# Performance work log

Hardware: AMD Instinct MI355X
Metric: run time of the kernel (lower is better)

Reference implementation:

```python
import jax, jax.numpy as jnp
import numpy as np

EMBED_DIM = 1024
NUM_HEADS = 16
HEAD_DIM = EMBED_DIM // NUM_HEADS
SEQ_LEN = 2048
BATCH = 2


def setup_inputs() -> dict:
    key = jax.random.key(0)
    ks = jax.random.split(key, 9)
    s = 1.0 / np.sqrt(EMBED_DIM)
    inputs = jax.random.normal(ks[0], (BATCH, SEQ_LEN, EMBED_DIM), dtype=jnp.float32)
    Wq = jax.random.uniform(ks[1], (EMBED_DIM, EMBED_DIM), jnp.float32, -s, s)
    bq = jax.random.uniform(ks[2], (EMBED_DIM,), jnp.float32, -s, s)
    Wk = jax.random.uniform(ks[3], (EMBED_DIM, EMBED_DIM), jnp.float32, -s, s)
    bk = jax.random.uniform(ks[4], (EMBED_DIM,), jnp.float32, -s, s)
    Wv = jax.random.uniform(ks[5], (EMBED_DIM, EMBED_DIM), jnp.float32, -s, s)
    bv = jax.random.uniform(ks[6], (EMBED_DIM,), jnp.float32, -s, s)
    Wo = jax.random.uniform(ks[7], (EMBED_DIM, EMBED_DIM), jnp.float32, -s, s)
    bo = jax.random.uniform(ks[8], (EMBED_DIM,), jnp.float32, -s, s)
    return {"inputs": inputs, "Wq": Wq, "bq": bq, "Wk": Wk, "bk": bk,
            "Wv": Wv, "bv": bv, "Wo": Wo, "bo": bo}


def reference(inputs, Wq, bq, Wk, bk, Wv, bv, Wo, bo):
    B, S, D = inputs.shape
    H, Hd = NUM_HEADS, HEAD_DIM

    def heads(x):  # [B,S,D] -> [B,H,S,Hd]
        return x.reshape(B, S, H, Hd).transpose(0, 2, 1, 3)

    q = heads(inputs @ Wq + bq)
    k = heads(inputs @ Wk + bk)
    v = heads(inputs @ Wv + bv)

    # [B,H,S,S] causal scores (naive, matching original module)
    scores = jnp.einsum('bhqd,bhkd->bhqk', q, k) * (Hd ** -0.5)
    causal = jnp.tril(jnp.ones((S, S), dtype=bool))
    scores = jnp.where(causal, scores, jnp.float32(-jnp.inf))
    attn = jax.nn.softmax(scores, axis=-1)

    out = jnp.einsum('bhqk,bhkd->bhqd', attn, v)
    out = out.transpose(0, 2, 1, 3).reshape(B, S, D)
    return out @ Wo + bo
```

## Files before the change

### kernel.cpp

```cpp
#include <hip/hip_runtime.h>
#include <stdint.h>
#include <stddef.h>

#define SEQ   2048
#define DIM   1024
#define NH    16
#define HD    64
#define MTOT  4096
#define LPAD  72
#define EPAD  136
#define FPAD  132

typedef __attribute__((ext_vector_type(8))) short short8;
typedef __attribute__((ext_vector_type(4))) float floatx4;
typedef __attribute__((ext_vector_type(16))) float floatx16;
typedef __attribute__((ext_vector_type(4))) float float4v;
typedef __attribute__((ext_vector_type(4))) unsigned short ushort4v;
typedef __attribute__((ext_vector_type(4))) unsigned int uint4v;

__device__ __forceinline__ floatx4 mfma_bf16(short8 a, short8 b, floatx4 c) {
    return __builtin_amdgcn_mfma_f32_16x16x32_bf16(a, b, c, 0, 0, 0);
}
__device__ __forceinline__ floatx16 mfma32(short8 a, short8 b, floatx16 c) {
    return __builtin_amdgcn_mfma_f32_32x32x16_bf16(a, b, c, 0, 0, 0);
}

__device__ __forceinline__ float b2f(unsigned short s) {
    unsigned int u = ((unsigned int)s) << 16;
    return __builtin_bit_cast(float, u);
}
__device__ __forceinline__ unsigned short f2b(float f) {
    unsigned int u = __builtin_bit_cast(unsigned int, f);
    u += 0x7fffu + ((u >> 16) & 1u);
    return (unsigned short)(u >> 16);
}
__device__ __forceinline__ unsigned int cvtpk(float lo, float hi) {
    unsigned int w;
    asm("v_cvt_pk_bf16_f32 %0, %1, %2" : "=v"(w) : "v"(lo), "v"(hi));
    return w;
}
__device__ __forceinline__ void swap32(unsigned int& a, unsigned int& b) {
    asm("v_permlane32_swap_b32 %0, %1" : "+v"(a), "+v"(b));
}
__device__ __forceinline__ short8 mk8(unsigned int a, unsigned int b,
                                      unsigned int c, unsigned int d) {
    uint4v u; u.x = a; u.y = b; u.z = c; u.w = d;
    return __builtin_bit_cast(short8, u);
}
__device__ __forceinline__ void g2l16(const unsigned short* g, unsigned short* l) {
    __builtin_amdgcn_global_load_lds(
        (const __attribute__((address_space(1))) void*)g,
        (__attribute__((address_space(3))) void*)l, 16, 0, 0);
}

__global__ __launch_bounds__(256) void cvt_f32_bf16(const float* __restrict__ in,
                                                    unsigned short* __restrict__ out) {
    const int i = (blockIdx.x * 256 + threadIdx.x) * 4;
    const float4v v = *(const float4v*)&in[i];
    ushort4v o;
    o.x = f2b(v.x); o.y = f2b(v.y); o.z = f2b(v.z); o.w = f2b(v.w);
    *(ushort4v*)&out[i] = o;
}

__global__ __launch_bounds__(256) void transpose_all(const float* __restrict__ w0,
                                                     const float* __restrict__ w1,
                                                     const float* __restrict__ w2,
                                                     const float* __restrict__ w3,
                                                     unsigned short* __restrict__ outbase) {
    __shared__ float t[64][65];
    const int z = blockIdx.z;
    const float* in = (z == 0) ? w0 : (z == 1) ? w1 : (z == 2) ? w2 : w3;
    unsigned short* out = outbase + (size_t)z * DIM * DIM;
    const int c0 = blockIdx.x * 64, r0 = blockIdx.y * 64;
    const int x = threadIdx.x, y = threadIdx.y;
#pragma unroll
    for (int i = 0; i < 64; i += 4)
        t[y + i][x] = in[(size_t)(r0 + y + i) * DIM + c0 + x];
    __syncthreads();
#pragma unroll
    for (int i = 0; i < 64; i += 4)
        out[(size_t)(c0 + y + i) * DIM + r0 + x] = f2b(t[x][y + i]);
}

__global__ __launch_bounds__(256) void gemm_fused(const unsigned short* __restrict__ A,
                                                  const unsigned short* __restrict__ WTbase,
                                                  const float* __restrict__ b0,
                                                  const float* __restrict__ b1,
                                                  const float* __restrict__ b2,
                                                  void* __restrict__ outbase,
                                                  int qkv) {
    __shared__ __attribute__((aligned(16))) unsigned short smem[2 * 128 * LPAD];
    unsigned short* As = smem;
    unsigned short* Bs = smem + 128 * 64;

    const int z = blockIdx.z;
    const unsigned short* BT = WTbase + (size_t)z * (DIM * DIM);
    const float* bias        = (z == 0) ? b0 : (z == 1) ? b1 : b2;
    const int mode = qkv ? ((z == 0) ? 1 : (z == 1) ? 3 : 4) : 0;
    float* Cf          = (float*)outbase;
    unsigned short* Cb = (unsigned short*)outbase + (size_t)z * ((size_t)MTOT * DIM);

    const int tid = threadIdx.x;
    const int w = tid >> 6, lane = tid & 63;
    const int quad = lane >> 4, l16 = lane & 15;
    const int wm = w >> 1, wn = w & 1;
    const int m0 = blockIdx.x * 128, n0 = blockIdx.y * 128;
    const int bb = m0 >> 11;

    floatx4 acc[4][4];
#pragma unroll
    for (int mi = 0; mi < 4; ++mi)
#pragma unroll
        for (int ni = 0; ni < 4; ++ni) acc[mi][ni] = (floatx4)0.0f;

    const int srow8 = lane >> 3;
    const int sgs8  = ((lane & 7) ^ srow8) * 8;
    const unsigned short* gA = &A [(size_t)(m0 + w * 8 + srow8) * DIM + sgs8];
    const unsigned short* gB = &BT[(size_t)(n0 + w * 8 + srow8) * DIM + sgs8];

    const int sx = l16 & 7;

    for (int k0 = 0; ; k0 += 64) {
#pragma unroll
        for (int i = 0; i < 4; ++i) {
            g2l16(gA + (size_t)i * (32 * DIM) + k0, &As[(i * 4 + w) * 512]);
            g2l16(gB + (size_t)i * (32 * DIM) + k0, &Bs[(i * 4 + w) * 512]);
        }
        __syncthreads();
#pragma unroll
        for (int kk = 0; kk < 2; ++kk) {
            short8 a[4], b[4];
#pragma unroll
            for (int mi = 0; mi < 4; ++mi)
                a[mi] = *(const short8*)&As[(wm * 64 + mi * 16 + l16) * 64 +
                                            (((kk * 4) + quad) ^ sx) * 8];
#pragma unroll
            for (int ni = 0; ni < 4; ++ni)
                b[ni] = *(const short8*)&Bs[(wn * 64 + ni * 16 + l16) * 64 +
                                            (((kk * 4) + quad) ^ sx) * 8];
#pragma unroll
            for (int mi = 0; mi < 4; ++mi)
#pragma unroll
                for (int ni = 0; ni < 4; ++ni)
                    acc[mi][ni] = mfma_bf16(a[mi], b[ni], acc[mi][ni]);
        }
        if (k0 + 64 >= DIM) break;
        __syncthreads();
    }

    float bvv[4];
#pragma unroll
    for (int ni = 0; ni < 4; ++ni) bvv[ni] = bias[n0 + wn * 64 + ni * 16 + l16];

    if (mode == 0) {
        float* T = (float*)smem;
        for (int p = 0; p < 4; ++p) {
            __syncthreads();
            if (wm == (p >> 1)) {
                const int mib = (p & 1) * 2;
#pragma unroll
                for (int mm = 0; mm < 2; ++mm)
#pragma unroll
                    for (int ni = 0; ni < 4; ++ni)
#pragma unroll
                        for (int r = 0; r < 4; ++r)
                            T[(mm * 16 + quad * 4 + r) * FPAD + wn * 64 + ni * 16 + l16] =
                                acc[mib + mm][ni][r] + bvv[ni];
            }
            __syncthreads();
#pragma unroll
            for (int it = 0; it < 4; ++it) {
                const int c = it * 256 + tid;
                const int row = c >> 5, nof = (c & 31) * 4;
                *(float4v*)&Cf[(size_t)(m0 + p * 32 + row) * DIM + n0 + nof] =
                    *(const float4v*)&T[row * FPAD + nof];
            }
        }
    } else if (mode == 1) {
        unsigned short* T = smem;
        __syncthreads();
#pragma unroll
        for (int mi = 0; mi < 4; ++mi)
#pragma unroll
            for (int ni = 0; ni < 4; ++ni)
#pragma unroll
                for (int r = 0; r < 4; ++r)
                    T[(wm * 64 + mi * 16 + quad * 4 + r) * EPAD + wn * 64 + ni * 16 + l16] =
                        f2b(acc[mi][ni][r] + bvv[ni]);
        __syncthreads();
#pragma unroll
        for (int it = 0; it < 8; ++it) {
            const int c = it * 256 + tid;
            const int seg = c >> 3, d8 = (c & 7) * 8;
            const int mm = seg >> 1, hseg = seg & 1;
            const int h = (n0 >> 6) + hseg;
            const int s = (m0 & (SEQ - 1)) + mm;
            *(short8*)&Cb[((size_t)(bb * NH + h) * SEQ + s) * HD + d8] =
                *(const short8*)&T[mm * EPAD + hseg * 64 + d8];
        }
    } else if (mode == 3) {
        unsigned short* T = smem;
        __syncthreads();
#pragma unroll
        for (int mi = 0; mi < 4; ++mi)
#pragma unroll
            for (int ni = 0; ni < 4; ++ni)
#pragma unroll
                for (int r = 0; r < 4; ++r)
                    T[(wm * 64 + mi * 16 + quad * 4 + r) * EPAD + wn * 64 + ni * 16 + l16] =
                        f2b(acc[mi][ni][r] + bvv[ni]);
        __syncthreads();
#pragma unroll
        for (int it = 0; it < 8; ++it) {
            const int f = it * 256 + tid;
            const int ln = f & 63, fragid = f >> 6;
            const int h2 = fragid >> 4;
            const int jb = (fragid >> 2) & 3;
            const int c  = fragid & 3;
            const short8 v = *(const short8*)&T[(jb * 32 + (ln & 31)) * EPAD +
                                                h2 * 64 + c * 16 + (ln >> 5) * 8];
            const int bh = bb * NH + (n0 >> 6) + h2;
            const int jg = ((m0 & (SEQ - 1)) >> 5) + jb;
            *(short8*)&Cb[(((size_t)bh * 64 + jg) * 4 + c) * 512 + ln * 8] = v;
        }
    } else {
        unsigned short* T = smem;
        __syncthreads();
#pragma unroll
        for (int mi = 0; mi < 4; ++mi)
#pragma unroll
            for (int ni = 0; ni < 4; ++ni) {
                ushort4v pk;
#pragma unroll
                for (int r = 0; r < 4; ++r) pk[r] = f2b(acc[mi][ni][r] + bvv[ni]);
                *(ushort4v*)&T[(wn * 64 + ni * 16 + l16) * EPAD + wm * 64 + mi * 16 + quad * 4] = pk;
            }
        __syncthreads();
#pragma unroll
        for (int it = 0; it < 8; ++it) {
            const int f = it * 256 + tid;
            const int ln = f & 63, fragid = f >> 6;
            const int h2 = fragid >> 4;
            const int jb = (fragid >> 2) & 3;
            const int dk = fragid & 3;
            const int d0 = dk >> 1, kk = dk & 1;
            const short8 v = *(const short8*)&T[(h2 * 64 + d0 * 32 + (ln & 31)) * EPAD +
                                                jb * 32 + kk * 16 + (ln >> 5) * 8];
            const int bh = bb * NH + (n0 >> 6) + h2;
            const int jg = ((m0 & (SEQ - 1)) >> 5) + jb;
            *(short8*)&Cb[(((size_t)bh * 64 + jg) * 4 + dk) * 512 + ln * 8] = v;
        }
    }
}

__global__ __launch_bounds__(256) void attn_fwd(const unsigned short* __restrict__ Q,
                                                const unsigned short* __restrict__ KP,
                                                const unsigned short* __restrict__ VP,
                                                unsigned short* __restrict__ O) {
    __shared__ float Fo[4][32][68];
    __shared__ float Fl[4][32];

    const int bh = blockIdx.x;
    const int qc = (gridDim.y - 1) - blockIdx.y;
    const int tid = threadIdx.x;
    const int w = tid >> 6, lane = tid & 63;
    const int ql  = lane & 31;
    const int hi  = lane >> 5;
    const int hi4 = hi * 4;
    const int hi8 = hi * 8;

    const unsigned short* Qh  = Q  + (size_t)bh * SEQ * HD;
    const unsigned short* KPh = KP + (size_t)bh * (64 * 2048);
    const unsigned short* VPh = VP + (size_t)bh * (64 * 2048);
    const int q0 = qc * 32;

    short8 qf[4];
#pragma unroll
    for (int c = 0; c < 4; ++c) {
        short8 t = *(const short8*)(Qh + (size_t)(q0 + ql) * HD + c * 16 + hi8);
        short8 o;
#pragma unroll
        for (int e = 0; e < 8; ++e)
            o[e] = (short)f2b(b2f((unsigned short)t[e]) * 0.125f);
        qf[c] = o;
    }

    floatx16 o_acc0 = (floatx16)0.0f, o_acc1 = (floatx16)0.0f;
    float l0 = 0.0f, l1 = 0.0f;

#define LOADKV(KF, VF, JJ) do {                                              \
        const unsigned short* kb_ = KPh + (size_t)(JJ) * 2048 + lane * 8;    \
        const unsigned short* vb_ = VPh + (size_t)(JJ) * 2048 + lane * 8;    \
        _Pragma("unroll")                                                    \
        for (int c_ = 0; c_ < 4; ++c_) {                                     \
            KF[c_] = *(const short8*)(kb_ + c_ * 512);                       \
            VF[c_] = *(const short8*)(vb_ + c_ * 512);                       \
        }                                                                    \
    } while (0)

#define ATT_BLOCK(KF, VF, MASKED) do {                                       \
        floatx16 st_ = (floatx16)0.0f;                                       \
        __builtin_amdgcn_s_setprio(1);                                       \
        _Pragma("unroll")                                                    \
        for (int c_ = 0; c_ < 4; ++c_) st_ = mfma32(KF[c_], qf[c_], st_);    \
        __builtin_amdgcn_s_setprio(0);                                       \
        float p_[16];                                                        \
        _Pragma("unroll")                                                    \
        for (int r_ = 0; r_ < 16; ++r_) {                                    \
            float e_ = __expf(st_[r_]);                                      \
            if (MASKED)                                                      \
                e_ = (((r_ & 3) + 8 * (r_ >> 2) + hi4) > ql) ? 0.0f : e_;    \
            p_[r_] = e_;                                                     \
        }                                                                    \
        l0 += (p_[0] + p_[1]) + (p_[2] + p_[3]);                             \
        l1 += (p_[4] + p_[5]) + (p_[6] + p_[7]);                             \
        l0 += (p_[8] + p_[9]) + (p_[10] + p_[11]);                           \
        l1 += (p_[12] + p_[13]) + (p_[14] + p_[15]);                         \
        unsigned int w0_ = cvtpk(p_[0], p_[1]),   w2_ = cvtpk(p_[4], p_[5]); \
        unsigned int w1_ = cvtpk(p_[2], p_[3]),   w3_ = cvtpk(p_[6], p_[7]); \
        unsigned int w4_ = cvtpk(p_[8], p_[9]),   w6_ = cvtpk(p_[12], p_[13]); \
        unsigned int w5_ = cvtpk(p_[10], p_[11]), w7_ = cvtpk(p_[14], p_[15]); \
        swap32(w0_, w2_); swap32(w1_, w3_);                                  \
        swap32(w4_, w6_); swap32(w5_, w7_);                                  \
        const short8 pa0_ = mk8(w0_, w1_, w2_, w3_);                         \
        const short8 pa1_ = mk8(w4_, w5_, w6_, w7_);                         \
        __builtin_amdgcn_s_setprio(1);                                       \
        o_acc0 = mfma32(pa0_, VF[0], o_acc0);                                \
        o_acc0 = mfma32(pa1_, VF[1], o_acc0);                                \
        o_acc1 = mfma32(pa0_, VF[2], o_acc1);                                \
        o_acc1 = mfma32(pa1_, VF[3], o_acc1);                                \
        __builtin_amdgcn_s_setprio(0);                                       \
    } while (0)

    short8 kfA[4], vfA[4], kfB[4], vfB[4];
    int j = w;
    if (j <= qc) {
        LOADKV(kfA, vfA, j);
        while (j + 8 <= qc) {
            LOADKV(kfB, vfB, j + 4);
            ATT_BLOCK(kfA, vfA, 0);
            LOADKV(kfA, vfA, j + 8);
            ATT_BLOCK(kfB, vfB, 0);
            j += 8;
        }
        if (j + 4 <= qc) {
            LOADKV(kfB, vfB, j + 4);
            ATT_BLOCK(kfA, vfA, 0);
            ATT_BLOCK(kfB, vfB, (j + 4) == qc);
        } else {
            ATT_BLOCK(kfA, vfA, j == qc);
        }
    }

    float* Fow = &Fo[w][0][0];
#pragma unroll
    for (int r = 0; r < 16; ++r) {
        const int row = (r & 3) + 8 * (r >> 2) + hi4;
        Fow[row * 68 + ql]      = o_acc0[r];
        Fow[row * 68 + 32 + ql] = o_acc1[r];
    }
    float l = l0 + l1;
    l += __shfl_xor(l, 32, 64);
    if (lane < 32) Fl[w][lane] = l;
    __syncthreads();

    const int rrow = w * 8 + (lane >> 3);
    const int c8   = (lane & 7) * 8;
    float s[8];
#pragma unroll
    for (int e = 0; e < 8; ++e) s[e] = 0.0f;
#pragma unroll
    for (int ww = 0; ww < 4; ++ww) {
        const float* src = &Fo[ww][rrow][c8];
        const float4v a = *(const float4v*)&src[0];
        const float4v b = *(const float4v*)&src[4];
        s[0] += a.x; s[1] += a.y; s[2] += a.z; s[3] += a.w;
        s[4] += b.x; s[5] += b.y; s[6] += b.z; s[7] += b.w;
    }
    const float lt = (Fl[0][rrow] + Fl[1][rrow]) + (Fl[2][rrow] + Fl[3][rrow]);
    const float iv = 1.0f / lt;
    const unsigned int o0 = cvtpk(s[0] * iv, s[1] * iv);
    const unsigned int o1 = cvtpk(s[2] * iv, s[3] * iv);
    const unsigned int o2 = cvtpk(s[4] * iv, s[5] * iv);
    const unsigned int o3 = cvtpk(s[6] * iv, s[7] * iv);
    const int bb = bh >> 4, h = bh & 15;
    *(short8*)&O[(size_t)(bb * SEQ + q0 + rrow) * DIM + h * HD + c8] =
        mk8(o0, o1, o2, o3);
#undef LOADKV
#undef ATT_BLOCK
}

extern "C" void kernel_launch(void* const* d_in, const int* in_sizes, int n_in,
                              void* d_out, int out_size, void* d_ws, size_t ws_size,
                              hipStream_t stream) {
    const float* X  = (const float*)d_in[0];
    const float* Wq = (const float*)d_in[1];
    const float* bq = (const float*)d_in[2];
    const float* Wk = (const float*)d_in[3];
    const float* bk = (const float*)d_in[4];
    const float* Wv = (const float*)d_in[5];
    const float* bv = (const float*)d_in[6];
    const float* Wo = (const float*)d_in[7];
    const float* bo = (const float*)d_in[8];

    unsigned short* ws = (unsigned short*)d_ws;
    const size_t WSZ = (size_t)DIM * DIM;
    const size_t TSZ = (size_t)MTOT * DIM;
    unsigned short* WqT = ws;
    unsigned short* WoT = ws + 3 * WSZ;
    unsigned short* Qb  = ws + 4 * WSZ;
    unsigned short* Kp  = Qb + TSZ;
    unsigned short* Vp  = Kp + TSZ;
    unsigned short* Ob  = Vp + TSZ;

    unsigned short* Xb = (unsigned short*)d_out;

    cvt_f32_bf16<<<dim3(TSZ / 1024), 256, 0, stream>>>(X, Xb);

    transpose_all<<<dim3(16, 16, 4), dim3(64, 4), 0, stream>>>(Wq, Wk, Wv, Wo, WqT);

    gemm_fused<<<dim3(MTOT / 128, DIM / 128, 3), 256, 0, stream>>>(
        Xb, WqT, bq, bk, bv, (void*)Qb, 1);

    attn_fwd<<<dim3(2 * NH, SEQ / 32), 256, 0, stream>>>(Qb, Kp, Vp, Ob);

    gemm_fused<<<dim3(MTOT / 128, DIM / 128, 1), 256, 0, stream>>>(
        Ob, WoT, bo, bo, bo, d_out, 0);
}
```

Before: 169.9 us.

## Pair causal query chunks per block and fold softmax scale into Q projection

Each attention block now handles two query chunks (qc and 63-qc) so every block does the same amount of causal work, and the grid shrinks to 32 in y. The 1/sqrt(d)*log2(e) scale is applied in the Q projection epilogue, which removes the per-element rescale and bf16 round trip at the start of attention, and exp is replaced by the raw v_exp_f32 (exp2) instruction. K/V pointers now advance incrementally. In exchange there are half as many blocks, extra syncthreads between the two chunks, and a slight change in rounding from scaling before the bf16 cast.

```diff
diff --git a/kernel.cpp b/kernel.cpp
--- a/kernel.cpp
+++ b/kernel.cpp
@@ -10,6 +10,7 @@
 #define LPAD  72
 #define EPAD  136
 #define FPAD  132
+#define QSCALE 0.18033688f
 
 typedef __attribute__((ext_vector_type(8))) short short8;
 typedef __attribute__((ext_vector_type(4))) float floatx4;
@@ -41,6 +42,11 @@
 }
 __device__ __forceinline__ void swap32(unsigned int& a, unsigned int& b) {
     asm("v_permlane32_swap_b32 %0, %1" : "+v"(a), "+v"(b));
+}
+__device__ __forceinline__ float exp2v(float x) {
+    float r;
+    asm("v_exp_f32 %0, %1" : "=v"(r) : "v"(x));
+    return r;
 }
 __device__ __forceinline__ short8 mk8(unsigned int a, unsigned int b,
                                       unsigned int c, unsigned int d) {
@@ -186,7 +192,7 @@
 #pragma unroll
                 for (int r = 0; r < 4; ++r)
                     T[(wm * 64 + mi * 16 + quad * 4 + r) * EPAD + wn * 64 + ni * 16 + l16] =
-                        f2b(acc[mi][ni][r] + bvv[ni]);
+                        f2b((acc[mi][ni][r] + bvv[ni]) * QSCALE);
         __syncthreads();
 #pragma unroll
         for (int it = 0; it < 8; ++it) {
@@ -261,7 +267,7 @@
     __shared__ float Fl[4][32];
 
     const int bh = blockIdx.x;
-    const int qc = (gridDim.y - 1) - blockIdx.y;
+    const int pr = blockIdx.y;
     const int tid = threadIdx.x;
     const int w = tid >> 6, lane = tid & 63;
     const int ql  = lane & 31;
@@ -272,30 +278,15 @@
     const unsigned short* Qh  = Q  + (size_t)bh * SEQ * HD;
     const unsigned short* KPh = KP + (size_t)bh * (64 * 2048);
     const unsigned short* VPh = VP + (size_t)bh * (64 * 2048);
-    const int q0 = qc * 32;
-
-    short8 qf[4];
-#pragma unroll
-    for (int c = 0; c < 4; ++c) {
-        short8 t = *(const short8*)(Qh + (size_t)(q0 + ql) * HD + c * 16 + hi8);
-        short8 o;
-#pragma unroll
-        for (int e = 0; e < 8; ++e)
-            o[e] = (short)f2b(b2f((unsigned short)t[e]) * 0.125f);
-        qf[c] = o;
-    }
-
-    floatx16 o_acc0 = (floatx16)0.0f, o_acc1 = (floatx16)0.0f;
-    float l0 = 0.0f, l1 = 0.0f;
-
-#define LOADKV(KF, VF, JJ) do {                                              \
-        const unsigned short* kb_ = KPh + (size_t)(JJ) * 2048 + lane * 8;    \
-        const unsigned short* vb_ = VPh + (size_t)(JJ) * 2048 + lane * 8;    \
+    const int bb = bh >> 4, h = bh & 15;
+
+#define LOADKV(KF, VF) do {                                                  \
         _Pragma("unroll")                                                    \
         for (int c_ = 0; c_ < 4; ++c_) {                                     \
-            KF[c_] = *(const short8*)(kb_ + c_ * 512);                       \
-            VF[c_] = *(const short8*)(vb_ + c_ * 512);                       \
+            KF[c_] = *(const short8*)(kp + c_ * 512);                        \
+            VF[c_] = *(const short8*)(vp + c_ * 512);                        \
         }                                                                    \
+        kp += 4 * 2048; vp += 4 * 2048;                                      \
     } while (0)
 
 #define ATT_BLOCK(KF, VF, MASKED) do {                                       \
@@ -307,7 +298,7 @@
         float p_[16];                                                        \
         _Pragma("unroll")                                                    \
         for (int r_ = 0; r_ < 16; ++r_) {                                    \
-            float e_ = __expf(st_[r_]);                                      \
+            float e_ = exp2v(st_[r_]);                                       \
             if (MASKED)                                                      \
                 e_ = (((r_ & 3) + 8 * (r_ >> 2) + hi4) > ql) ? 0.0f : e_;    \
             p_[r_] = e_;                                                     \
@@ -332,60 +323,79 @@
         __builtin_amdgcn_s_setprio(0);                                       \
     } while (0)
 
-    short8 kfA[4], vfA[4], kfB[4], vfB[4];
-    int j = w;
-    if (j <= qc) {
-        LOADKV(kfA, vfA, j);
-        while (j + 8 <= qc) {
-            LOADKV(kfB, vfB, j + 4);
-            ATT_BLOCK(kfA, vfA, 0);
-            LOADKV(kfA, vfA, j + 8);
-            ATT_BLOCK(kfB, vfB, 0);
-            j += 8;
-        }
-        if (j + 4 <= qc) {
-            LOADKV(kfB, vfB, j + 4);
-            ATT_BLOCK(kfA, vfA, 0);
-            ATT_BLOCK(kfB, vfB, (j + 4) == qc);
-        } else {
-            ATT_BLOCK(kfA, vfA, j == qc);
-        }
+#pragma unroll 1
+    for (int t = 0; t < 2; ++t) {
+        const int qc = t ? pr : (63 - pr);
+        const int q0 = qc * 32;
+
+        short8 qf[4];
+#pragma unroll
+        for (int c = 0; c < 4; ++c)
+            qf[c] = *(const short8*)(Qh + (size_t)(q0 + ql) * HD + c * 16 + hi8);
+
+        floatx16 o_acc0 = (floatx16)0.0f, o_acc1 = (floatx16)0.0f;
+        float l0 = 0.0f, l1 = 0.0f;
+
+        const int n = (qc >= w) ? ((qc - w) >> 2) + 1 : 0;
+        const bool lastmask = ((qc & 3) == w);
+        const unsigned short* kp = KPh + (size_t)w * 2048 + lane * 8;
+        const unsigned short* vp = VPh + (size_t)w * 2048 + lane * 8;
+
+        if (n > 0) {
+            short8 kfA[4], vfA[4], kfB[4], vfB[4];
+            LOADKV(kfA, vfA);
+            int b = 0;
+            while (b + 2 <= n - 1) {
+                LOADKV(kfB, vfB);
+                ATT_BLOCK(kfA, vfA, 0);
+                LOADKV(kfA, vfA);
+                ATT_BLOCK(kfB, vfB, 0);
+                b += 2;
+            }
+            if (b == n - 2) {
+                LOADKV(kfB, vfB);
+                ATT_BLOCK(kfA, vfA, 0);
+                ATT_BLOCK(kfB, vfB, lastmask);
+            } else {
+                ATT_BLOCK(kfA, vfA, lastmask);
+            }
+        }
+
+        float* Fow = &Fo[w][0][0];
+#pragma unroll
+        for (int r = 0; r < 16; ++r) {
+            const int row = (r & 3) + 8 * (r >> 2) + hi4;
+            Fow[row * 68 + ql]      = o_acc0[r];
+            Fow[row * 68 + 32 + ql] = o_acc1[r];
+        }
+        float l = l0 + l1;
+        l += __shfl_xor(l, 32, 64);
+        if (lane < 32) Fl[w][lane] = l;
+        __syncthreads();
+
+        const int rrow = w * 8 + (lane >> 3);
+        const int c8   = (lane & 7) * 8;
+        float s[8];
+#pragma unroll
+        for (int e = 0; e < 8; ++e) s[e] = 0.0f;
+#pragma unroll
+        for (int ww = 0; ww < 4; ++ww) {
+            const float* src = &Fo[ww][rrow][c8];
+            const float4v a = *(const float4v*)&src[0];
+            const float4v b2 = *(const float4v*)&src[4];
+            s[0] += a.x;  s[1] += a.y;  s[2] += a.z;  s[3] += a.w;
+            s[4] += b2.x; s[5] += b2.y; s[6] += b2.z; s[7] += b2.w;
+        }
+        const float lt = (Fl[0][rrow] + Fl[1][rrow]) + (Fl[2][rrow] + Fl[3][rrow]);
+        const float iv = 1.0f / lt;
+        const unsigned int o0 = cvtpk(s[0] * iv, s[1] * iv);
+        const unsigned int o1 = cvtpk(s[2] * iv, s[3] * iv);
+        const unsigned int o2 = cvtpk(s[4] * iv, s[5] * iv);
+        const unsigned int o3 = cvtpk(s[6] * iv, s[7] * iv);
+        *(short8*)&O[(size_t)(bb * SEQ + q0 + rrow) * DIM + h * HD + c8] =
+            mk8(o0, o1, o2, o3);
+        __syncthreads();
     }
-
-    float* Fow = &Fo[w][0][0];
-#pragma unroll
-    for (int r = 0; r < 16; ++r) {
-        const int row = (r & 3) + 8 * (r >> 2) + hi4;
-        Fow[row * 68 + ql]      = o_acc0[r];
-        Fow[row * 68 + 32 + ql] = o_acc1[r];
-    }
-    float l = l0 + l1;
-    l += __shfl_xor(l, 32, 64);
-    if (lane < 32) Fl[w][lane] = l;
-    __syncthreads();
-
-    const int rrow = w * 8 + (lane >> 3);
-    const int c8   = (lane & 7) * 8;
-    float s[8];
-#pragma unroll
-    for (int e = 0; e < 8; ++e) s[e] = 0.0f;
-#pragma unroll
-    for (int ww = 0; ww < 4; ++ww) {
-        const float* src = &Fo[ww][rrow][c8];
-        const float4v a = *(const float4v*)&src[0];
-        const float4v b = *(const float4v*)&src[4];
-        s[0] += a.x; s[1] += a.y; s[2] += a.z; s[3] += a.w;
-        s[4] += b.x; s[5] += b.y; s[6] += b.z; s[7] += b.w;
-    }
-    const float lt = (Fl[0][rrow] + Fl[1][rrow]) + (Fl[2][rrow] + Fl[3][rrow]);
-    const float iv = 1.0f / lt;
-    const unsigned int o0 = cvtpk(s[0] * iv, s[1] * iv);
-    const unsigned int o1 = cvtpk(s[2] * iv, s[3] * iv);
-    const unsigned int o2 = cvtpk(s[4] * iv, s[5] * iv);
-    const unsigned int o3 = cvtpk(s[6] * iv, s[7] * iv);
-    const int bb = bh >> 4, h = bh & 15;
-    *(short8*)&O[(size_t)(bb * SEQ + q0 + rrow) * DIM + h * HD + c8] =
-        mk8(o0, o1, o2, o3);
 #undef LOADKV
 #undef ATT_BLOCK
 }
@@ -422,7 +432,7 @@
     gemm_fused<<<dim3(MTOT / 128, DIM / 128, 3), 256, 0, stream>>>(
         Xb, WqT, bq, bk, bv, (void*)Qb, 1);
 
-    attn_fwd<<<dim3(2 * NH, SEQ / 32), 256, 0, stream>>>(Qb, Kp, Vp, Ob);
+    attn_fwd<<<dim3(2 * NH, 32), 256, 0, stream>>>(Qb, Kp, Vp, Ob);
 
     gemm_fused<<<dim3(MTOT / 128, DIM / 128, 1), 256, 0, stream>>>(
         Ob, WoT, bo, bo, bo, d_out, 0);
```

Result: no change. 170.9 us (+0.6%).
